# Performance work log

Measured on AMD Instinct MI355X. Metric: run time of the kernel, lower is better.

Reference implementation:

```python
import jax, jax.numpy as jnp
import numpy as np

N, E = 2048, 65536
EMBED, H0, H1 = 64, 128, 128
VOCAB = 625  # 5**k with k=4
SLOPE = 0.01  # F.leaky_relu_ default negative slope


def setup_inputs() -> dict:
    key = jax.random.key(0)
    ks = jax.random.split(key, 20)
    f = jax.random.normal
    return {
        "node_ids": jax.random.randint(ks[0], (N,), 0, VOCAB),
        "edge_index": jax.random.randint(ks[1], (2, E), 0, N),
        "edge_attr": jax.random.uniform(ks[2], (E, 1), dtype=jnp.float32),
        "m": (jax.random.uniform(ks[3], (N, N)) > 0.5).astype(jnp.float32),
        "emb": f(ks[4], (VOCAB, EMBED), dtype=jnp.float32) * 0.1,
        "l0_lin1": f(ks[5], (H0, EMBED + 1), dtype=jnp.float32) * 0.1,
        "l0_lin2": f(ks[6], (H0, H0), dtype=jnp.float32) * 0.1,
        "l0_att_l": f(ks[7], (H0,), dtype=jnp.float32) * 0.1,
        "l0_att_r": f(ks[8], (EMBED,), dtype=jnp.float32) * 0.1,
        "l0_bias": f(ks[9], (H0,), dtype=jnp.float32) * 0.1,
        "l1_lin1": f(ks[10], (H1, H0 + 1), dtype=jnp.float32) * 0.1,
        "l1_lin2": f(ks[11], (H1, H1), dtype=jnp.float32) * 0.1,
        "l1_att_l": f(ks[12], (H1,), dtype=jnp.float32) * 0.1,
        "l1_att_r": f(ks[13], (H0,), dtype=jnp.float32) * 0.1,
        "l1_bias": f(ks[14], (H1,), dtype=jnp.float32) * 0.1,
        "W1": f(ks[15], (20, (EMBED + H0 + H1) * 2), dtype=jnp.float32) * 0.1,
        "b1": f(ks[16], (20,), dtype=jnp.float32) * 0.1,
        "W2": f(ks[17], (20,), dtype=jnp.float32) * 0.1,
        "b2": f(ks[18], (1,), dtype=jnp.float32) * 0.1,
    }


def _segment_softmax(alpha, index, n):
    # numerically-stable softmax over edges grouped by destination node
    amax = jax.ops.segment_max(alpha, index, num_segments=n)
    amax = jnp.where(jnp.isfinite(amax), amax, 0.0)
    e = jnp.exp(alpha - amax[index])
    denom = jax.ops.segment_sum(e, index, num_segments=n)
    return e / (denom[index] + 1e-16)


def _gate_conv(x, src, dst, edge_attr, lin1, lin2, att_l, att_r, bias, n):
    # PyG AttentiveFP GATEConv: message = lin2(leaky_relu(lin1([x_j, e]))) * alpha
    h = jax.nn.leaky_relu(jnp.concatenate([x[src], edge_attr], axis=-1) @ lin1.T, SLOPE)  # [E,out]
    alpha = jax.nn.leaky_relu(h @ att_l + x[dst] @ att_r, SLOPE)  # [E]
    alpha = _segment_softmax(alpha, dst, n)
    msg = (h @ lin2.T) * alpha[:, None]
    return jax.ops.segment_sum(msg, dst, num_segments=n) + bias


def reference(node_ids, edge_index, edge_attr, m, emb,
              l0_lin1, l0_lin2, l0_att_l, l0_att_r, l0_bias,
              l1_lin1, l1_lin2, l1_att_l, l1_att_r, l1_bias,
              W1, b1, W2, b2):
    src, dst = edge_index[0], edge_index[1]
    x = emb[node_ids]  # [N, EMBED]
    h1 = jax.nn.relu(_gate_conv(x, src, dst, edge_attr, l0_lin1, l0_lin2, l0_att_l, l0_att_r, l0_bias, N))
    h2 = jax.nn.relu(_gate_conv(h1, src, dst, edge_attr, l1_lin1, l1_lin2, l1_att_l, l1_att_r, l1_bias, N))
    feat = jnp.concatenate([x, h1, h2], axis=-1)  # [N, C], C = EMBED+H0+H1
    C = feat.shape[-1]
    # 1x1 conv over concat([x_i, x_j]) == split linear: out[c,i,j] = W1[c,:C]@feat[i] + W1[c,C:]@feat[j] + b1[c]
    a = feat @ W1[:, :C].T  # [N, 20] row (i) term
    b = feat @ W1[:, C:].T  # [N, 20] col (j) term
    h = jax.nn.relu(a[:, None, :] + b[None, :, :] + b1)  # [N, N, 20]
    logits = (h @ W2 + b2[0]) * m  # [N, N]; mask multiplies logits as in original
    return jax.nn.softmax(logits, axis=1)
```

## Files before the change

### kernel.cpp

```cpp
#include <hip/hip_runtime.h>
#include <math.h>

#define N 2048
#define E 65536
#define EMBED 64
#define H 128
#define NT 20
#define C3 320
#define CAP 96
#define SLOPE 0.01f

__device__ __forceinline__ float leaky(float x) { return x > 0.f ? x : SLOPE * x; }

__device__ __forceinline__ float wave_sum(float v) {
#pragma unroll
    for (int o = 32; o > 0; o >>= 1) v += __shfl_xor(v, o, 64);
    return v;
}

__global__ __launch_bounds__(256) void k_prep(
    const int* __restrict__ ei, const float* __restrict__ eattr,
    int* __restrict__ cursor, int* __restrict__ srcs, float* __restrict__ eas,
    const float* __restrict__ l1_lin1, float* __restrict__ WT1,
    const float* __restrict__ l0_lin2, float* __restrict__ LT0,
    const float* __restrict__ l1_lin2, float* __restrict__ LT1,
    const int* __restrict__ ids, const float* __restrict__ emb,
    const float* __restrict__ l0_lin1,
    float* __restrict__ x, float* __restrict__ A) {
    int b = blockIdx.x;
    int tid = threadIdx.x;
    if (b < 256) {
        int e = b * 256 + tid;
        int d = ei[E + e];
        int pos = atomicAdd(&cursor[d], 1);
        if (pos < CAP) {
            srcs[d * CAP + pos] = ei[e];
            eas[d * CAP + pos] = eattr[e];
        }
    } else if (b < 448) {
        int j = (b - 256) * 256 + tid;
        if (j < 16384) {
            int c = j >> 7, k = j & 127;
            WT1[j] = l1_lin1[k * (H + 1) + c];
        } else if (j < 32768) {
            int jj = j - 16384; int c = jj >> 7, k = jj & 127;
            LT0[jj] = l0_lin2[k * H + c];
        } else {
            int jj = j - 32768; int c = jj >> 7, k = jj & 127;
            LT1[jj] = l1_lin2[k * H + c];
        }
    } else {
        __shared__ float lw[EMBED][130];
        int n0 = (b - 448) * 8;
        for (int j = tid; j < H * (EMBED + 1); j += 256) {
            int k = j / (EMBED + 1), c = j % (EMBED + 1);
            float v = l0_lin1[j];
            if (c < EMBED) lw[c][k] = v;
        }
        for (int idx = tid; idx < 8 * EMBED; idx += 256) {
            int g = idx >> 6, c = idx & 63;
            x[(n0 + g) * EMBED + c] = emb[ids[n0 + g] * EMBED + c];
        }
        __syncthreads();
        int k = tid & 127, half = tid >> 7;
        const float* xr[4];
#pragma unroll
        for (int it = 0; it < 4; it++) {
            int nn = __builtin_amdgcn_readfirstlane(n0 + 2 * it + half);
            xr[it] = emb + (size_t)ids[nn] * EMBED;
        }
        float acc[4] = {0.f, 0.f, 0.f, 0.f};
#pragma unroll 4
        for (int c = 0; c < EMBED; c++) {
            float wt = lw[c][k];
#pragma unroll
            for (int it = 0; it < 4; it++) acc[it] = fmaf(xr[it][c], wt, acc[it]);
        }
#pragma unroll
        for (int it = 0; it < 4; it++) A[(n0 + 2 * it + half) * H + k] = acc[it];
    }
}

__device__ __forceinline__ void gate_wave(
    int dst, int lane, float xr,
    const float* __restrict__ A,
    float w0, float w1, float attl0, float attl1,
    const int* __restrict__ srcs, const float* __restrict__ eas, int cnt,
    float& out0, float& out1) {
    int c0 = 2 * lane;
    int base = dst * CAP;
    float mmax = -INFINITY, s = 0.f, v0 = 0.f, v1 = 0.f;
    for (int i0 = 0; i0 < cnt; i0 += 8) {
        int nb = cnt - i0; if (nb > 8) nb = 8;
        float h0[8], h1[8], p[8];
#pragma unroll
        for (int e = 0; e < 8; e++) {
            float ea = 0.f; float2 av = make_float2(0.f, 0.f);
            if (e < nb) {
                int sn = srcs[base + i0 + e];
                ea = eas[base + i0 + e];
                av = *(const float2*)&A[sn * H + c0];
            }
            h0[e] = leaky(fmaf(w0, ea, av.x));
            h1[e] = leaky(fmaf(w1, ea, av.y));
            p[e] = h0[e] * attl0 + h1[e] * attl1;
        }
#pragma unroll
        for (int o = 32; o > 0; o >>= 1) {
#pragma unroll
            for (int e = 0; e < 8; e++) p[e] += __shfl_xor(p[e], o, 64);
        }
        float alpha[8];
#pragma unroll
        for (int e = 0; e < 8; e++)
            alpha[e] = (e < nb) ? leaky(p[e] + xr) : -INFINITY;
        float mb = alpha[0];
#pragma unroll
        for (int e = 1; e < 8; e++) mb = fmaxf(mb, alpha[e]);
        float mnew = fmaxf(mmax, mb);
        float scale = __expf(mmax - mnew);
        float sw = 0.f, sv0 = 0.f, sv1 = 0.f;
#pragma unroll
        for (int e = 0; e < 8; e++) {
            float we = __expf(alpha[e] - mnew);
            sw += we;
            sv0 = fmaf(we, h0[e], sv0);
            sv1 = fmaf(we, h1[e], sv1);
        }
        s = fmaf(s, scale, sw);
        v0 = fmaf(v0, scale, sv0);
        v1 = fmaf(v1, scale, sv1);
        mmax = mnew;
    }
    float inv = 1.f / (s + 1e-16f);
    out0 = v0 * inv;
    out1 = v1 * inv;
}

__global__ __launch_bounds__(512) void k_g0(
    const float* __restrict__ x, const float* __restrict__ A0,
    const float* __restrict__ l0_lin1,
    const float* __restrict__ att_l, const float* __restrict__ att_r,
    const int* __restrict__ srcs, const float* __restrict__ eas,
    const int* __restrict__ cursor,
    const float* __restrict__ LT0, const float* __restrict__ b0,
    const float* __restrict__ WT1,
    float* __restrict__ h1, float* __restrict__ A1) {
    __shared__ float agg_s[8][H];
    __shared__ float hs[8][H];
    int n0 = blockIdx.x * 8;
    int tid = threadIdx.x;
    int wv = __builtin_amdgcn_readfirstlane(tid >> 6);
    int lane = tid & 63;
    int c0 = 2 * lane;

    int dst = n0 + wv;
    float xr = wave_sum(x[dst * EMBED + lane] * att_r[lane]);
    float attl0 = att_l[c0], attl1 = att_l[c0 + 1];
    float w0 = l0_lin1[c0 * (EMBED + 1) + EMBED];
    float w1 = l0_lin1[(c0 + 1) * (EMBED + 1) + EMBED];
    int cnt = cursor[dst]; if (cnt > CAP) cnt = CAP;

    float o0, o1;
    gate_wave(dst, lane, xr, A0, w0, w1, attl0, attl1, srcs, eas, cnt, o0, o1);
    agg_s[wv][c0] = o0;
    agg_s[wv][c0 + 1] = o1;
    __syncthreads();

    int k = tid & 127, q = tid >> 7;
    float bk = b0[k];
    float acc0 = bk, acc1 = bk;
#pragma unroll 2
    for (int ct = 0; ct < H / 4; ct++) {
        float u0 = LT0[(4 * ct + 0) * H + k];
        float u1 = LT0[(4 * ct + 1) * H + k];
        float u2 = LT0[(4 * ct + 2) * H + k];
        float u3 = LT0[(4 * ct + 3) * H + k];
        float4 f0 = *(const float4*)&agg_s[q][4 * ct];
        float4 f1 = *(const float4*)&agg_s[q + 4][4 * ct];
        acc0 = fmaf(f0.x, u0, acc0); acc0 = fmaf(f0.y, u1, acc0);
        acc0 = fmaf(f0.z, u2, acc0); acc0 = fmaf(f0.w, u3, acc0);
        acc1 = fmaf(f1.x, u0, acc1); acc1 = fmaf(f1.y, u1, acc1);
        acc1 = fmaf(f1.z, u2, acc1); acc1 = fmaf(f1.w, u3, acc1);
    }
    float hv0 = fmaxf(acc0, 0.f), hv1 = fmaxf(acc1, 0.f);
    h1[(n0 + q) * H + k] = hv0;
    h1[(n0 + q + 4) * H + k] = hv1;
    hs[q][k] = hv0;
    hs[q + 4][k] = hv1;
    __syncthreads();

    float a0 = 0.f, a1 = 0.f;
#pragma unroll 2
    for (int ct = 0; ct < H / 4; ct++) {
        float u0 = WT1[(4 * ct + 0) * H + k];
        float u1 = WT1[(4 * ct + 1) * H + k];
        float u2 = WT1[(4 * ct + 2) * H + k];
        float u3 = WT1[(4 * ct + 3) * H + k];
        float4 f0 = *(const float4*)&hs[q][4 * ct];
        float4 f1 = *(const float4*)&hs[q + 4][4 * ct];
        a0 = fmaf(f0.x, u0, a0); a0 = fmaf(f0.y, u1, a0);
        a0 = fmaf(f0.z, u2, a0); a0 = fmaf(f0.w, u3, a0);
        a1 = fmaf(f1.x, u0, a1); a1 = fmaf(f1.y, u1, a1);
        a1 = fmaf(f1.z, u2, a1); a1 = fmaf(f1.w, u3, a1);
    }
    A1[(n0 + q) * H + k] = a0;
    A1[(n0 + q + 4) * H + k] = a1;
}

__global__ __launch_bounds__(512) void k_g1(
    const float* __restrict__ h1g, const float* __restrict__ A1,
    const float* __restrict__ l1_lin1,
    const float* __restrict__ att_l, const float* __restrict__ att_r,
    const int* __restrict__ srcs, const float* __restrict__ eas,
    const int* __restrict__ cursor,
    const float* __restrict__ LT1, const float* __restrict__ bL1,
    const float* __restrict__ x, const float* __restrict__ W1,
    float* __restrict__ aArr, float* __restrict__ bT) {
    __shared__ float agg_s[8][H];
    __shared__ float feat[8][C3];
    int n0 = blockIdx.x * 8;
    int tid = threadIdx.x;
    int wv = __builtin_amdgcn_readfirstlane(tid >> 6);
    int lane = tid & 63;
    int c0 = 2 * lane;

    int dst = n0 + wv;
    float xr = wave_sum(h1g[dst * H + lane] * att_r[lane] +
                        h1g[dst * H + 64 + lane] * att_r[64 + lane]);
    float attl0 = att_l[c0], attl1 = att_l[c0 + 1];
    float w0 = l1_lin1[c0 * (H + 1) + H];
    float w1 = l1_lin1[(c0 + 1) * (H + 1) + H];
    int cnt = cursor[dst]; if (cnt > CAP) cnt = CAP;

    float o0, o1;
    gate_wave(dst, lane, xr, A1, w0, w1, attl0, attl1, srcs, eas, cnt, o0, o1);
    agg_s[wv][c0] = o0;
    agg_s[wv][c0 + 1] = o1;

    for (int idx = tid; idx < 8 * EMBED; idx += 512) {
        int g = idx >> 6, c = idx & 63;
        feat[g][c] = x[(n0 + g) * EMBED + c];
    }
    for (int idx = tid; idx < 8 * H; idx += 512) {
        int g = idx >> 7, c = idx & 127;
        feat[g][EMBED + c] = h1g[(n0 + g) * H + c];
    }
    __syncthreads();

    int k = tid & 127, q = tid >> 7;
    float bk = bL1[k];
    float acc0 = bk, acc1 = bk;
#pragma unroll 2
    for (int ct = 0; ct < H / 4; ct++) {
        float u0 = LT1[(4 * ct + 0) * H + k];
        float u1 = LT1[(4 * ct + 1) * H + k];
        float u2 = LT1[(4 * ct + 2) * H + k];
        float u3 = LT1[(4 * ct + 3) * H + k];
        float4 f0 = *(const float4*)&agg_s[q][4 * ct];
        float4 f1 = *(const float4*)&agg_s[q + 4][4 * ct];
        acc0 = fmaf(f0.x, u0, acc0); acc0 = fmaf(f0.y, u1, acc0);
        acc0 = fmaf(f0.z, u2, acc0); acc0 = fmaf(f0.w, u3, acc0);
        acc1 = fmaf(f1.x, u0, acc1); acc1 = fmaf(f1.y, u1, acc1);
        acc1 = fmaf(f1.z, u2, acc1); acc1 = fmaf(f1.w, u3, acc1);
    }
    feat[q][EMBED + H + k] = fmaxf(acc0, 0.f);
    feat[q + 4][EMBED + H + k] = fmaxf(acc1, 0.f);
    __syncthreads();

    if (tid < 320) {
        int g = tid / 40, u = tid % 40;
        int t = u % 20, side = u / 20;
        const float* wrow = W1 + t * (2 * C3) + side * C3;
        float s = 0.f;
#pragma unroll 4
        for (int ct = 0; ct < C3 / 4; ct++) {
            float4 fv = *(const float4*)&feat[g][4 * ct];
            float4 wv4 = *(const float4*)&wrow[4 * ct];
            s = fmaf(fv.x, wv4.x, s);
            s = fmaf(fv.y, wv4.y, s);
            s = fmaf(fv.z, wv4.z, s);
            s = fmaf(fv.w, wv4.w, s);
        }
        if (side == 0) aArr[(n0 + g) * NT + t] = s;
        else bT[t * N + (n0 + g)] = s;
    }
}

__global__ __launch_bounds__(256) void k_final(const float* __restrict__ aArr,
                                               const float* __restrict__ bT,
                                               const float* __restrict__ b1,
                                               const float* __restrict__ W2,
                                               const float* __restrict__ b2,
                                               const float* __restrict__ mmat,
                                               float* __restrict__ out) {
    __shared__ float red[16];
    int i0 = blockIdx.x * 4;
    int tid = threadIdx.x;
    int lane = tid & 63, wv = tid >> 6;
    float w2r[NT];
#pragma unroll
    for (int t = 0; t < NT; t++) w2r[t] = W2[t];
    float b2v = b2[0];
    float ab[4][NT];
#pragma unroll
    for (int g = 0; g < 4; g++) {
#pragma unroll
        for (int t = 0; t < NT; t++)
            ab[g][t] = aArr[(i0 + g) * NT + t] + b1[t];
    }
    float l[4][8];
    float tmax[4] = {-INFINITY, -INFINITY, -INFINITY, -INFINITY};
#pragma unroll
    for (int it = 0; it < 8; it++) {
        int j = tid + 256 * it;
        float bt[NT];
#pragma unroll
        for (int t = 0; t < NT; t++) bt[t] = bT[t * N + j];
#pragma unroll
        for (int g = 0; g < 4; g++) {
            float s = b2v;
#pragma unroll
            for (int t = 0; t < NT; t++)
                s += fmaxf(ab[g][t] + bt[t], 0.f) * w2r[t];
            s *= mmat[(size_t)(i0 + g) * N + j];
            l[g][it] = s;
            tmax[g] = fmaxf(tmax[g], s);
        }
    }
#pragma unroll
    for (int g = 0; g < 4; g++) {
#pragma unroll
        for (int o = 32; o > 0; o >>= 1)
            tmax[g] = fmaxf(tmax[g], __shfl_xor(tmax[g], o, 64));
    }
    if (lane == 0) {
#pragma unroll
        for (int g = 0; g < 4; g++) red[wv * 4 + g] = tmax[g];
    }
    __syncthreads();
    float mfin[4];
#pragma unroll
    for (int g = 0; g < 4; g++)
        mfin[g] = fmaxf(fmaxf(red[g], red[4 + g]), fmaxf(red[8 + g], red[12 + g]));
    __syncthreads();

    float ts[4] = {0.f, 0.f, 0.f, 0.f};
#pragma unroll
    for (int it = 0; it < 8; it++) {
#pragma unroll
        for (int g = 0; g < 4; g++) {
            float e = __expf(l[g][it] - mfin[g]);
            l[g][it] = e;
            ts[g] += e;
        }
    }
#pragma unroll
    for (int g = 0; g < 4; g++) {
#pragma unroll
        for (int o = 32; o > 0; o >>= 1) ts[g] += __shfl_xor(ts[g], o, 64);
    }
    if (lane == 0) {
#pragma unroll
        for (int g = 0; g < 4; g++) red[wv * 4 + g] = ts[g];
    }
    __syncthreads();
    float inv[4];
#pragma unroll
    for (int g = 0; g < 4; g++)
        inv[g] = 1.f / (red[g] + red[4 + g] + red[8 + g] + red[12 + g]);

#pragma unroll
    for (int it = 0; it < 8; it++) {
        int j = tid + 256 * it;
#pragma unroll
        for (int g = 0; g < 4; g++)
            out[(size_t)(i0 + g) * N + j] = l[g][it] * inv[g];
    }
}

extern "C" void kernel_launch(void* const* d_in, const int* in_sizes, int n_in,
                              void* d_out, int out_size, void* d_ws, size_t ws_size,
                              hipStream_t stream) {
    const int*   node_ids = (const int*)d_in[0];
    const int*   ei       = (const int*)d_in[1];
    const float* eattr    = (const float*)d_in[2];
    const float* mmat     = (const float*)d_in[3];
    const float* emb      = (const float*)d_in[4];
    const float* l0_lin1  = (const float*)d_in[5];
    const float* l0_lin2  = (const float*)d_in[6];
    const float* l0_att_l = (const float*)d_in[7];
    const float* l0_att_r = (const float*)d_in[8];
    const float* l0_bias  = (const float*)d_in[9];
    const float* l1_lin1  = (const float*)d_in[10];
    const float* l1_lin2  = (const float*)d_in[11];
    const float* l1_att_l = (const float*)d_in[12];
    const float* l1_att_r = (const float*)d_in[13];
    const float* l1_bias  = (const float*)d_in[14];
    const float* W1       = (const float*)d_in[15];
    const float* b1       = (const float*)d_in[16];
    const float* W2       = (const float*)d_in[17];
    const float* b2       = (const float*)d_in[18];
    float* out = (float*)d_out;

    char* w = (char*)d_ws;
    auto alloc = [&](size_t bytes) {
        char* p = w;
        w += (bytes + 255) & ~(size_t)255;
        return p;
    };
    int*   cursor = (int*)alloc(N * sizeof(int));
    int*   srcs   = (int*)alloc(N * CAP * sizeof(int));
    float* eas    = (float*)alloc(N * CAP * sizeof(float));
    float* x      = (float*)alloc(N * EMBED * sizeof(float));
    float* A0     = (float*)alloc(N * H * sizeof(float));
    float* A1     = (float*)alloc(N * H * sizeof(float));
    float* h1     = (float*)alloc(N * H * sizeof(float));
    float* aArr   = (float*)alloc(N * NT * sizeof(float));
    float* bT     = (float*)alloc(NT * N * sizeof(float));
    float* WT1    = (float*)alloc(H * H * sizeof(float));
    float* LT0    = (float*)alloc(H * H * sizeof(float));
    float* LT1    = (float*)alloc(H * H * sizeof(float));

    hipMemsetAsync(cursor, 0, N * sizeof(int), stream);

    k_prep<<<704, 256, 0, stream>>>(ei, eattr, cursor, srcs, eas,
                                    l1_lin1, WT1, l0_lin2, LT0, l1_lin2, LT1,
                                    node_ids, emb, l0_lin1, x, A0);
    k_g0<<<N / 8, 512, 0, stream>>>(x, A0, l0_lin1, l0_att_l, l0_att_r,
                                    srcs, eas, cursor, LT0, l0_bias, WT1, h1, A1);
    k_g1<<<N / 8, 512, 0, stream>>>(h1, A1, l1_lin1, l1_att_l, l1_att_r,
                                    srcs, eas, cursor, LT1, l1_bias, x, W1, aArr, bT);
    k_final<<<N / 4, 256, 0, stream>>>(aArr, bT, b1, W2, b2, mmat, out);
}
```

Before: 185.8 us.

## Fuse all four kernels into one persistent kernel with software grid barriers

Replaces the prep, two gate-conv and final softmax kernels with a single 256-block persistent kernel. The stages are separated by atomic-counter grid barriers in global memory, and shared memory is reused across phases. The aim is to remove launch overhead and inter-kernel gaps. The trade-off is that only 256 blocks run, which may underfill the GPU in the final softmax phase (k_final used 512 blocks of 256 threads). Correctness also depends on all blocks being co-resident for the spin barrier.

```diff
diff --git a/kernel.cpp b/kernel.cpp
--- a/kernel.cpp
+++ b/kernel.cpp
@@ -9,6 +9,8 @@
 #define C3 320
 #define CAP 96
 #define SLOPE 0.01f
+#define NBLK 256
+#define NTHR 512
 
 __device__ __forceinline__ float leaky(float x) { return x > 0.f ? x : SLOPE * x; }
 
@@ -18,67 +20,16 @@
     return v;
 }
 
-__global__ __launch_bounds__(256) void k_prep(
-    const int* __restrict__ ei, const float* __restrict__ eattr,
-    int* __restrict__ cursor, int* __restrict__ srcs, float* __restrict__ eas,
-    const float* __restrict__ l1_lin1, float* __restrict__ WT1,
-    const float* __restrict__ l0_lin2, float* __restrict__ LT0,
-    const float* __restrict__ l1_lin2, float* __restrict__ LT1,
-    const int* __restrict__ ids, const float* __restrict__ emb,
-    const float* __restrict__ l0_lin1,
-    float* __restrict__ x, float* __restrict__ A) {
-    int b = blockIdx.x;
-    int tid = threadIdx.x;
-    if (b < 256) {
-        int e = b * 256 + tid;
-        int d = ei[E + e];
-        int pos = atomicAdd(&cursor[d], 1);
-        if (pos < CAP) {
-            srcs[d * CAP + pos] = ei[e];
-            eas[d * CAP + pos] = eattr[e];
-        }
-    } else if (b < 448) {
-        int j = (b - 256) * 256 + tid;
-        if (j < 16384) {
-            int c = j >> 7, k = j & 127;
-            WT1[j] = l1_lin1[k * (H + 1) + c];
-        } else if (j < 32768) {
-            int jj = j - 16384; int c = jj >> 7, k = jj & 127;
-            LT0[jj] = l0_lin2[k * H + c];
-        } else {
-            int jj = j - 32768; int c = jj >> 7, k = jj & 127;
-            LT1[jj] = l1_lin2[k * H + c];
-        }
-    } else {
-        __shared__ float lw[EMBED][130];
-        int n0 = (b - 448) * 8;
-        for (int j = tid; j < H * (EMBED + 1); j += 256) {
-            int k = j / (EMBED + 1), c = j % (EMBED + 1);
-            float v = l0_lin1[j];
-            if (c < EMBED) lw[c][k] = v;
-        }
-        for (int idx = tid; idx < 8 * EMBED; idx += 256) {
-            int g = idx >> 6, c = idx & 63;
-            x[(n0 + g) * EMBED + c] = emb[ids[n0 + g] * EMBED + c];
-        }
-        __syncthreads();
-        int k = tid & 127, half = tid >> 7;
-        const float* xr[4];
-#pragma unroll
-        for (int it = 0; it < 4; it++) {
-            int nn = __builtin_amdgcn_readfirstlane(n0 + 2 * it + half);
-            xr[it] = emb + (size_t)ids[nn] * EMBED;
-        }
-        float acc[4] = {0.f, 0.f, 0.f, 0.f};
-#pragma unroll 4
-        for (int c = 0; c < EMBED; c++) {
-            float wt = lw[c][k];
-#pragma unroll
-            for (int it = 0; it < 4; it++) acc[it] = fmaf(xr[it][c], wt, acc[it]);
-        }
-#pragma unroll
-        for (int it = 0; it < 4; it++) A[(n0 + 2 * it + half) * H + k] = acc[it];
-    }
+__device__ __forceinline__ void grid_sync(int* bar, int target) {
+    __syncthreads();
+    if (threadIdx.x == 0) {
+        __builtin_amdgcn_fence(__ATOMIC_RELEASE, "agent");
+        __hip_atomic_fetch_add(bar, 1, __ATOMIC_RELAXED, __HIP_MEMORY_SCOPE_AGENT);
+        while (__hip_atomic_load(bar, __ATOMIC_RELAXED, __HIP_MEMORY_SCOPE_AGENT) < target)
+            __builtin_amdgcn_s_sleep(2);
+        __builtin_amdgcn_fence(__ATOMIC_ACQUIRE, "agent");
+    }
+    __syncthreads();
 }
 
 __device__ __forceinline__ void gate_wave(
@@ -92,7 +43,7 @@
     float mmax = -INFINITY, s = 0.f, v0 = 0.f, v1 = 0.f;
     for (int i0 = 0; i0 < cnt; i0 += 8) {
         int nb = cnt - i0; if (nb > 8) nb = 8;
-        float h0[8], h1[8], p[8];
+        float h0[8], h1v[8], p[8];
 #pragma unroll
         for (int e = 0; e < 8; e++) {
             float ea = 0.f; float2 av = make_float2(0.f, 0.f);
@@ -102,8 +53,8 @@
                 av = *(const float2*)&A[sn * H + c0];
             }
             h0[e] = leaky(fmaf(w0, ea, av.x));
-            h1[e] = leaky(fmaf(w1, ea, av.y));
-            p[e] = h0[e] * attl0 + h1[e] * attl1;
+            h1v[e] = leaky(fmaf(w1, ea, av.y));
+            p[e] = h0[e] * attl0 + h1v[e] * attl1;
         }
 #pragma unroll
         for (int o = 32; o > 0; o >>= 1) {
@@ -125,7 +76,7 @@
             float we = __expf(alpha[e] - mnew);
             sw += we;
             sv0 = fmaf(we, h0[e], sv0);
-            sv1 = fmaf(we, h1[e], sv1);
+            sv1 = fmaf(we, h1v[e], sv1);
         }
         s = fmaf(s, scale, sw);
         v0 = fmaf(v0, scale, sv0);
@@ -137,245 +88,292 @@
     out1 = v1 * inv;
 }
 
-__global__ __launch_bounds__(512) void k_g0(
-    const float* __restrict__ x, const float* __restrict__ A0,
-    const float* __restrict__ l0_lin1,
-    const float* __restrict__ att_l, const float* __restrict__ att_r,
-    const int* __restrict__ srcs, const float* __restrict__ eas,
-    const int* __restrict__ cursor,
-    const float* __restrict__ LT0, const float* __restrict__ b0,
-    const float* __restrict__ WT1,
-    float* __restrict__ h1, float* __restrict__ A1) {
-    __shared__ float agg_s[8][H];
-    __shared__ float hs[8][H];
-    int n0 = blockIdx.x * 8;
-    int tid = threadIdx.x;
-    int wv = __builtin_amdgcn_readfirstlane(tid >> 6);
-    int lane = tid & 63;
-    int c0 = 2 * lane;
-
-    int dst = n0 + wv;
-    float xr = wave_sum(x[dst * EMBED + lane] * att_r[lane]);
-    float attl0 = att_l[c0], attl1 = att_l[c0 + 1];
-    float w0 = l0_lin1[c0 * (EMBED + 1) + EMBED];
-    float w1 = l0_lin1[(c0 + 1) * (EMBED + 1) + EMBED];
-    int cnt = cursor[dst]; if (cnt > CAP) cnt = CAP;
-
-    float o0, o1;
-    gate_wave(dst, lane, xr, A0, w0, w1, attl0, attl1, srcs, eas, cnt, o0, o1);
-    agg_s[wv][c0] = o0;
-    agg_s[wv][c0 + 1] = o1;
-    __syncthreads();
-
-    int k = tid & 127, q = tid >> 7;
-    float bk = b0[k];
-    float acc0 = bk, acc1 = bk;
+__global__ __launch_bounds__(NTHR) void k_fused(
+    const int* __restrict__ ids, const int* __restrict__ ei,
+    const float* __restrict__ eattr, const float* __restrict__ mmat,
+    const float* __restrict__ emb,
+    const float* __restrict__ l0_lin1, const float* __restrict__ l0_lin2,
+    const float* __restrict__ l0_att_l, const float* __restrict__ l0_att_r,
+    const float* __restrict__ l0_bias,
+    const float* __restrict__ l1_lin1, const float* __restrict__ l1_lin2,
+    const float* __restrict__ l1_att_l, const float* __restrict__ l1_att_r,
+    const float* __restrict__ l1_bias,
+    const float* __restrict__ W1, const float* __restrict__ b1,
+    const float* __restrict__ W2, const float* __restrict__ b2,
+    int* __restrict__ cursor, int* __restrict__ bar,
+    int* __restrict__ srcs, float* __restrict__ eas,
+    float* __restrict__ x, float* __restrict__ A0, float* __restrict__ A1,
+    float* __restrict__ h1, float* __restrict__ aArr, float* __restrict__ bT,
+    float* __restrict__ WT1, float* __restrict__ LT0, float* __restrict__ LT1,
+    float* __restrict__ out) {
+    __shared__ float smem[EMBED * 130];
+    const int b = blockIdx.x;
+    const int tid = threadIdx.x;
+    const int gtid = b * NTHR + tid;
+
+    if (gtid < E) {
+        int d = ei[E + gtid];
+        int pos = atomicAdd(&cursor[d], 1);
+        if (pos < CAP) {
+            srcs[d * CAP + pos] = ei[gtid];
+            eas[d * CAP + pos] = eattr[gtid];
+        }
+    } else if (gtid < E + 16384) {
+        int j = gtid - E;
+        WT1[j] = l1_lin1[(j & 127) * (H + 1) + (j >> 7)];
+    } else if (gtid < E + 32768) {
+        int j = gtid - (E + 16384);
+        LT0[j] = l0_lin2[(j & 127) * H + (j >> 7)];
+    } else if (gtid < E + 49152) {
+        int j = gtid - (E + 32768);
+        LT1[j] = l1_lin2[(j & 127) * H + (j >> 7)];
+    }
+    {
+        int g = gtid >> 6, c = gtid & 63;
+        x[gtid] = emb[ids[g] * EMBED + c];
+    }
+    {
+        float (*lw)[130] = (float(*)[130])smem;
+        for (int j = tid; j < H * (EMBED + 1); j += NTHR) {
+            int kk = j / (EMBED + 1), c = j % (EMBED + 1);
+            float v = l0_lin1[j];
+            if (c < EMBED) lw[c][kk] = v;
+        }
+        __syncthreads();
+        int n0 = b * 8;
+        int k = tid & 127, grp = tid >> 7;
+        int nnA = __builtin_amdgcn_readfirstlane(n0 + grp);
+        int nnB = __builtin_amdgcn_readfirstlane(n0 + grp + 4);
+        const float* xrA = emb + (size_t)ids[nnA] * EMBED;
+        const float* xrB = emb + (size_t)ids[nnB] * EMBED;
+        float accA = 0.f, accB = 0.f;
+#pragma unroll 4
+        for (int c = 0; c < EMBED; c++) {
+            float wt = lw[c][k];
+            accA = fmaf(xrA[c], wt, accA);
+            accB = fmaf(xrB[c], wt, accB);
+        }
+        A0[(n0 + grp) * H + k] = accA;
+        A0[(n0 + grp + 4) * H + k] = accB;
+    }
+    grid_sync(bar, NBLK);
+
+    {
+        float (*agg_s)[H] = (float(*)[H])smem;
+        float (*hs)[H] = (float(*)[H])(smem + 8 * H);
+        int n0 = b * 8;
+        int wv = __builtin_amdgcn_readfirstlane(tid >> 6);
+        int lane = tid & 63;
+        int c0 = 2 * lane;
+        int dst = n0 + wv;
+        float xr = wave_sum(x[dst * EMBED + lane] * l0_att_r[lane]);
+        float attl0 = l0_att_l[c0], attl1 = l0_att_l[c0 + 1];
+        float w0 = l0_lin1[c0 * (EMBED + 1) + EMBED];
+        float w1 = l0_lin1[(c0 + 1) * (EMBED + 1) + EMBED];
+        int cnt = cursor[dst]; if (cnt > CAP) cnt = CAP;
+
+        float o0, o1;
+        gate_wave(dst, lane, xr, A0, w0, w1, attl0, attl1, srcs, eas, cnt, o0, o1);
+        agg_s[wv][c0] = o0;
+        agg_s[wv][c0 + 1] = o1;
+        __syncthreads();
+
+        int k = tid & 127, q = tid >> 7;
+        float bk = l0_bias[k];
+        float acc0 = bk, acc1 = bk;
 #pragma unroll 2
-    for (int ct = 0; ct < H / 4; ct++) {
-        float u0 = LT0[(4 * ct + 0) * H + k];
-        float u1 = LT0[(4 * ct + 1) * H + k];
-        float u2 = LT0[(4 * ct + 2) * H + k];
-        float u3 = LT0[(4 * ct + 3) * H + k];
-        float4 f0 = *(const float4*)&agg_s[q][4 * ct];
-        float4 f1 = *(const float4*)&agg_s[q + 4][4 * ct];
-        acc0 = fmaf(f0.x, u0, acc0); acc0 = fmaf(f0.y, u1, acc0);
-        acc0 = fmaf(f0.z, u2, acc0); acc0 = fmaf(f0.w, u3, acc0);
-        acc1 = fmaf(f1.x, u0, acc1); acc1 = fmaf(f1.y, u1, acc1);
-        acc1 = fmaf(f1.z, u2, acc1); acc1 = fmaf(f1.w, u3, acc1);
-    }
-    float hv0 = fmaxf(acc0, 0.f), hv1 = fmaxf(acc1, 0.f);
-    h1[(n0 + q) * H + k] = hv0;
-    h1[(n0 + q + 4) * H + k] = hv1;
-    hs[q][k] = hv0;
-    hs[q + 4][k] = hv1;
-    __syncthreads();
-
-    float a0 = 0.f, a1 = 0.f;
+        for (int ct = 0; ct < H / 4; ct++) {
+            float u0 = LT0[(4 * ct + 0) * H + k];
+            float u1 = LT0[(4 * ct + 1) * H + k];
+            float u2 = LT0[(4 * ct + 2) * H + k];
+            float u3 = LT0[(4 * ct + 3) * H + k];
+            float4 f0 = *(const float4*)&agg_s[q][4 * ct];
+            float4 f1 = *(const float4*)&agg_s[q + 4][4 * ct];
+            acc0 = fmaf(f0.x, u0, acc0); acc0 = fmaf(f0.y, u1, acc0);
+            acc0 = fmaf(f0.z, u2, acc0); acc0 = fmaf(f0.w, u3, acc0);
+            acc1 = fmaf(f1.x, u0, acc1); acc1 = fmaf(f1.y, u1, acc1);
+            acc1 = fmaf(f1.z, u2, acc1); acc1 = fmaf(f1.w, u3, acc1);
+        }
+        float hv0 = fmaxf(acc0, 0.f), hv1 = fmaxf(acc1, 0.f);
+        h1[(n0 + q) * H + k] = hv0;
+        h1[(n0 + q + 4) * H + k] = hv1;
+        hs[q][k] = hv0;
+        hs[q + 4][k] = hv1;
+        __syncthreads();
+
+        float a0 = 0.f, a1 = 0.f;
 #pragma unroll 2
-    for (int ct = 0; ct < H / 4; ct++) {
-        float u0 = WT1[(4 * ct + 0) * H + k];
-        float u1 = WT1[(4 * ct + 1) * H + k];
-        float u2 = WT1[(4 * ct + 2) * H + k];
-        float u3 = WT1[(4 * ct + 3) * H + k];
-        float4 f0 = *(const float4*)&hs[q][4 * ct];
-        float4 f1 = *(const float4*)&hs[q + 4][4 * ct];
-        a0 = fmaf(f0.x, u0, a0); a0 = fmaf(f0.y, u1, a0);
-        a0 = fmaf(f0.z, u2, a0); a0 = fmaf(f0.w, u3, a0);
-        a1 = fmaf(f1.x, u0, a1); a1 = fmaf(f1.y, u1, a1);
-        a1 = fmaf(f1.z, u2, a1); a1 = fmaf(f1.w, u3, a1);
-    }
-    A1[(n0 + q) * H + k] = a0;
-    A1[(n0 + q + 4) * H + k] = a1;
-}
-
-__global__ __launch_bounds__(512) void k_g1(
-    const float* __restrict__ h1g, const float* __restrict__ A1,
-    const float* __restrict__ l1_lin1,
-    const float* __restrict__ att_l, const float* __restrict__ att_r,
-    const int* __restrict__ srcs, const float* __restrict__ eas,
-    const int* __restrict__ cursor,
-    const float* __restrict__ LT1, const float* __restrict__ bL1,
-    const float* __restrict__ x, const float* __restrict__ W1,
-    float* __restrict__ aArr, float* __restrict__ bT) {
-    __shared__ float agg_s[8][H];
-    __shared__ float feat[8][C3];
-    int n0 = blockIdx.x * 8;
-    int tid = threadIdx.x;
-    int wv = __builtin_amdgcn_readfirstlane(tid >> 6);
-    int lane = tid & 63;
-    int c0 = 2 * lane;
-
-    int dst = n0 + wv;
-    float xr = wave_sum(h1g[dst * H + lane] * att_r[lane] +
-                        h1g[dst * H + 64 + lane] * att_r[64 + lane]);
-    float attl0 = att_l[c0], attl1 = att_l[c0 + 1];
-    float w0 = l1_lin1[c0 * (H + 1) + H];
-    float w1 = l1_lin1[(c0 + 1) * (H + 1) + H];
-    int cnt = cursor[dst]; if (cnt > CAP) cnt = CAP;
-
-    float o0, o1;
-    gate_wave(dst, lane, xr, A1, w0, w1, attl0, attl1, srcs, eas, cnt, o0, o1);
-    agg_s[wv][c0] = o0;
-    agg_s[wv][c0 + 1] = o1;
-
-    for (int idx = tid; idx < 8 * EMBED; idx += 512) {
-        int g = idx >> 6, c = idx & 63;
-        feat[g][c] = x[(n0 + g) * EMBED + c];
-    }
-    for (int idx = tid; idx < 8 * H; idx += 512) {
-        int g = idx >> 7, c = idx & 127;
-        feat[g][EMBED + c] = h1g[(n0 + g) * H + c];
-    }
-    __syncthreads();
-
-    int k = tid & 127, q = tid >> 7;
-    float bk = bL1[k];
-    float acc0 = bk, acc1 = bk;
+        for (int ct = 0; ct < H / 4; ct++) {
+            float u0 = WT1[(4 * ct + 0) * H + k];
+            float u1 = WT1[(4 * ct + 1) * H + k];
+            float u2 = WT1[(4 * ct + 2) * H + k];
+            float u3 = WT1[(4 * ct + 3) * H + k];
+            float4 f0 = *(const float4*)&hs[q][4 * ct];
+            float4 f1 = *(const float4*)&hs[q + 4][4 * ct];
+            a0 = fmaf(f0.x, u0, a0); a0 = fmaf(f0.y, u1, a0);
+            a0 = fmaf(f0.z, u2, a0); a0 = fmaf(f0.w, u3, a0);
+            a1 = fmaf(f1.x, u0, a1); a1 = fmaf(f1.y, u1, a1);
+            a1 = fmaf(f1.z, u2, a1); a1 = fmaf(f1.w, u3, a1);
+        }
+        A1[(n0 + q) * H + k] = a0;
+        A1[(n0 + q + 4) * H + k] = a1;
+    }
+    grid_sync(bar, 2 * NBLK);
+
+    {
+        float (*agg_s)[H] = (float(*)[H])smem;
+        float (*feat)[C3] = (float(*)[C3])(smem + 8 * H);
+        int n0 = b * 8;
+        int wv = __builtin_amdgcn_readfirstlane(tid >> 6);
+        int lane = tid & 63;
+        int c0 = 2 * lane;
+        int dst = n0 + wv;
+        float xr = wave_sum(h1[dst * H + lane] * l1_att_r[lane] +
+                            h1[dst * H + 64 + lane] * l1_att_r[64 + lane]);
+        float attl0 = l1_att_l[c0], attl1 = l1_att_l[c0 + 1];
+        float w0 = l1_lin1[c0 * (H + 1) + H];
+        float w1 = l1_lin1[(c0 + 1) * (H + 1) + H];
+        int cnt = cursor[dst]; if (cnt > CAP) cnt = CAP;
+
+        float o0, o1;
+        gate_wave(dst, lane, xr, A1, w0, w1, attl0, attl1, srcs, eas, cnt, o0, o1);
+        agg_s[wv][c0] = o0;
+        agg_s[wv][c0 + 1] = o1;
+
+        for (int idx = tid; idx < 8 * EMBED; idx += NTHR) {
+            int g = idx >> 6, c = idx & 63;
+            feat[g][c] = x[(n0 + g) * EMBED + c];
+        }
+        for (int idx = tid; idx < 8 * H; idx += NTHR) {
+            int g = idx >> 7, c = idx & 127;
+            feat[g][EMBED + c] = h1[(n0 + g) * H + c];
+        }
+        __syncthreads();
+
+        int k = tid & 127, q = tid >> 7;
+        float bk = l1_bias[k];
+        float acc0 = bk, acc1 = bk;
 #pragma unroll 2
-    for (int ct = 0; ct < H / 4; ct++) {
-        float u0 = LT1[(4 * ct + 0) * H + k];
-        float u1 = LT1[(4 * ct + 1) * H + k];
-        float u2 = LT1[(4 * ct + 2) * H + k];
-        float u3 = LT1[(4 * ct + 3) * H + k];
-        float4 f0 = *(const float4*)&agg_s[q][4 * ct];
-        float4 f1 = *(const float4*)&agg_s[q + 4][4 * ct];
-        acc0 = fmaf(f0.x, u0, acc0); acc0 = fmaf(f0.y, u1, acc0);
-        acc0 = fmaf(f0.z, u2, acc0); acc0 = fmaf(f0.w, u3, acc0);
-        acc1 = fmaf(f1.x, u0, acc1); acc1 = fmaf(f1.y, u1, acc1);
-        acc1 = fmaf(f1.z, u2, acc1); acc1 = fmaf(f1.w, u3, acc1);
-    }
-    feat[q][EMBED + H + k] = fmaxf(acc0, 0.f);
-    feat[q + 4][EMBED + H + k] = fmaxf(acc1, 0.f);
-    __syncthreads();
-
-    if (tid < 320) {
-        int g = tid / 40, u = tid % 40;
-        int t = u % 20, side = u / 20;
-        const float* wrow = W1 + t * (2 * C3) + side * C3;
-        float s = 0.f;
+        for (int ct = 0; ct < H / 4; ct++) {
+            float u0 = LT1[(4 * ct + 0) * H + k];
+            float u1 = LT1[(4 * ct + 1) * H + k];
+            float u2 = LT1[(4 * ct + 2) * H + k];
+            float u3 = LT1[(4 * ct + 3) * H + k];
+            float4 f0 = *(const float4*)&agg_s[q][4 * ct];
+            float4 f1 = *(const float4*)&agg_s[q + 4][4 * ct];
+            acc0 = fmaf(f0.x, u0, acc0); acc0 = fmaf(f0.y, u1, acc0);
+            acc0 = fmaf(f0.z, u2, acc0); acc0 = fmaf(f0.w, u3, acc0);
+            acc1 = fmaf(f1.x, u0, acc1); acc1 = fmaf(f1.y, u1, acc1);
+            acc1 = fmaf(f1.z, u2, acc1); acc1 = fmaf(f1.w, u3, acc1);
+        }
+        feat[q][EMBED + H + k] = fmaxf(acc0, 0.f);
+        feat[q + 4][EMBED + H + k] = fmaxf(acc1, 0.f);
+        __syncthreads();
+
+        if (tid < 320) {
+            int g = tid / 40, u = tid % 40;
+            int t = u % 20, side = u / 20;
+            const float* wrow = W1 + t * (2 * C3) + side * C3;
+            float s = 0.f;
 #pragma unroll 4
-        for (int ct = 0; ct < C3 / 4; ct++) {
-            float4 fv = *(const float4*)&feat[g][4 * ct];
-            float4 wv4 = *(const float4*)&wrow[4 * ct];
-            s = fmaf(fv.x, wv4.x, s);
-            s = fmaf(fv.y, wv4.y, s);
-            s = fmaf(fv.z, wv4.z, s);
-            s = fmaf(fv.w, wv4.w, s);
-        }
-        if (side == 0) aArr[(n0 + g) * NT + t] = s;
-        else bT[t * N + (n0 + g)] = s;
-    }
-}
-
-__global__ __launch_bounds__(256) void k_final(const float* __restrict__ aArr,
-                                               const float* __restrict__ bT,
-                                               const float* __restrict__ b1,
-                                               const float* __restrict__ W2,
-                                               const float* __restrict__ b2,
-                                               const float* __restrict__ mmat,
-                                               float* __restrict__ out) {
-    __shared__ float red[16];
-    int i0 = blockIdx.x * 4;
-    int tid = threadIdx.x;
-    int lane = tid & 63, wv = tid >> 6;
-    float w2r[NT];
-#pragma unroll
-    for (int t = 0; t < NT; t++) w2r[t] = W2[t];
-    float b2v = b2[0];
-    float ab[4][NT];
-#pragma unroll
-    for (int g = 0; g < 4; g++) {
-#pragma unroll
-        for (int t = 0; t < NT; t++)
-            ab[g][t] = aArr[(i0 + g) * NT + t] + b1[t];
-    }
-    float l[4][8];
-    float tmax[4] = {-INFINITY, -INFINITY, -INFINITY, -INFINITY};
-#pragma unroll
-    for (int it = 0; it < 8; it++) {
-        int j = tid + 256 * it;
-        float bt[NT];
-#pragma unroll
-        for (int t = 0; t < NT; t++) bt[t] = bT[t * N + j];
+            for (int ct = 0; ct < C3 / 4; ct++) {
+                float4 fv = *(const float4*)&feat[g][4 * ct];
+                float4 wv4 = *(const float4*)&wrow[4 * ct];
+                s = fmaf(fv.x, wv4.x, s);
+                s = fmaf(fv.y, wv4.y, s);
+                s = fmaf(fv.z, wv4.z, s);
+                s = fmaf(fv.w, wv4.w, s);
+            }
+            if (side == 0) aArr[(n0 + g) * NT + t] = s;
+            else bT[t * N + (n0 + g)] = s;
+        }
+    }
+    grid_sync(bar, 3 * NBLK);
+
+    {
+        float* red = smem + (tid >> 8) * 16;
+        int t256 = tid & 255;
+        int i0 = b * 8 + (tid >> 8) * 4;
+        int lane = t256 & 63, wv = t256 >> 6;
+        float w2r[NT];
+#pragma unroll
+        for (int t = 0; t < NT; t++) w2r[t] = W2[t];
+        float b2v = b2[0];
+        float ab[4][NT];
 #pragma unroll
         for (int g = 0; g < 4; g++) {
-            float s = b2v;
 #pragma unroll
             for (int t = 0; t < NT; t++)
-                s += fmaxf(ab[g][t] + bt[t], 0.f) * w2r[t];
-            s *= mmat[(size_t)(i0 + g) * N + j];
-            l[g][it] = s;
-            tmax[g] = fmaxf(tmax[g], s);
-        }
-    }
-#pragma unroll
-    for (int g = 0; g < 4; g++) {
-#pragma unroll
-        for (int o = 32; o > 0; o >>= 1)
-            tmax[g] = fmaxf(tmax[g], __shfl_xor(tmax[g], o, 64));
-    }
-    if (lane == 0) {
-#pragma unroll
-        for (int g = 0; g < 4; g++) red[wv * 4 + g] = tmax[g];
-    }
-    __syncthreads();
-    float mfin[4];
-#pragma unroll
-    for (int g = 0; g < 4; g++)
-        mfin[g] = fmaxf(fmaxf(red[g], red[4 + g]), fmaxf(red[8 + g], red[12 + g]));
-    __syncthreads();
-
-    float ts[4] = {0.f, 0.f, 0.f, 0.f};
-#pragma unroll
-    for (int it = 0; it < 8; it++) {
+                ab[g][t] = aArr[(i0 + g) * NT + t] + b1[t];
+        }
+        float l[4][8];
+        float tmax[4] = {-INFINITY, -INFINITY, -INFINITY, -INFINITY};
+#pragma unroll
+        for (int it = 0; it < 8; it++) {
+            int j = t256 + 256 * it;
+            float bt[NT];
+#pragma unroll
+            for (int t = 0; t < NT; t++) bt[t] = bT[t * N + j];
+#pragma unroll
+            for (int g = 0; g < 4; g++) {
+                float s = b2v;
+#pragma unroll
+                for (int t = 0; t < NT; t++)
+                    s += fmaxf(ab[g][t] + bt[t], 0.f) * w2r[t];
+                s *= mmat[(size_t)(i0 + g) * N + j];
+                l[g][it] = s;
+                tmax[g] = fmaxf(tmax[g], s);
+            }
+        }
 #pragma unroll
         for (int g = 0; g < 4; g++) {
-            float e = __expf(l[g][it] - mfin[g]);
-            l[g][it] = e;
-            ts[g] += e;
-        }
-    }
-#pragma unroll
-    for (int g = 0; g < 4; g++) {
-#pragma unroll
-        for (int o = 32; o > 0; o >>= 1) ts[g] += __shfl_xor(ts[g], o, 64);
-    }
-    if (lane == 0) {
-#pragma unroll
-        for (int g = 0; g < 4; g++) red[wv * 4 + g] = ts[g];
-    }
-    __syncthreads();
-    float inv[4];
-#pragma unroll
-    for (int g = 0; g < 4; g++)
-        inv[g] = 1.f / (red[g] + red[4 + g] + red[8 + g] + red[12 + g]);
-
-#pragma unroll
-    for (int it = 0; it < 8; it++) {
-        int j = tid + 256 * it;
+#pragma unroll
+            for (int o = 32; o > 0; o >>= 1)
+                tmax[g] = fmaxf(tmax[g], __shfl_xor(tmax[g], o, 64));
+        }
+        if (lane == 0) {
+#pragma unroll
+            for (int g = 0; g < 4; g++) red[wv * 4 + g] = tmax[g];
+        }
+        __syncthreads();
+        float mfin[4];
 #pragma unroll
         for (int g = 0; g < 4; g++)
-            out[(size_t)(i0 + g) * N + j] = l[g][it] * inv[g];
+            mfin[g] = fmaxf(fmaxf(red[g], red[4 + g]), fmaxf(red[8 + g], red[12 + g]));
+        __syncthreads();
+
+        float ts[4] = {0.f, 0.f, 0.f, 0.f};
+#pragma unroll
+        for (int it = 0; it < 8; it++) {
+#pragma unroll
+            for (int g = 0; g < 4; g++) {
+                float e = __expf(l[g][it] - mfin[g]);
+                l[g][it] = e;
+                ts[g] += e;
+            }
+        }
+#pragma unroll
+        for (int g = 0; g < 4; g++) {
+#pragma unroll
+            for (int o = 32; o > 0; o >>= 1) ts[g] += __shfl_xor(ts[g], o, 64);
+        }
+        if (lane == 0) {
+#pragma unroll
+            for (int g = 0; g < 4; g++) red[wv * 4 + g] = ts[g];
+        }
+        __syncthreads();
+        float inv[4];
+#pragma unroll
+        for (int g = 0; g < 4; g++)
+            inv[g] = 1.f / (red[g] + red[4 + g] + red[8 + g] + red[12 + g]);
+
+#pragma unroll
+        for (int it = 0; it < 8; it++) {
+            int j = t256 + 256 * it;
+#pragma unroll
+            for (int g = 0; g < 4; g++)
+                out[(size_t)(i0 + g) * N + j] = l[g][it] * inv[g];
+        }
     }
 }
 
@@ -409,7 +407,8 @@
         w += (bytes + 255) & ~(size_t)255;
         return p;
     };
-    int*   cursor = (int*)alloc(N * sizeof(int));
+    int*   cursor = (int*)alloc((N + 64) * sizeof(int));
+    int*   bar    = cursor + N;
     int*   srcs   = (int*)alloc(N * CAP * sizeof(int));
     float* eas    = (float*)alloc(N * CAP * sizeof(float));
     float* x      = (float*)alloc(N * EMBED * sizeof(float));
@@ -422,14 +421,12 @@
     float* LT0    = (float*)alloc(H * H * sizeof(float));
     float* LT1    = (float*)alloc(H * H * sizeof(float));
 
-    hipMemsetAsync(cursor, 0, N * sizeof(int), stream);
-
-    k_prep<<<704, 256, 0, stream>>>(ei, eattr, cursor, srcs, eas,
-                                    l1_lin1, WT1, l0_lin2, LT0, l1_lin2, LT1,
-                                    node_ids, emb, l0_lin1, x, A0);
-    k_g0<<<N / 8, 512, 0, stream>>>(x, A0, l0_lin1, l0_att_l, l0_att_r,
-                                    srcs, eas, cursor, LT0, l0_bias, WT1, h1, A1);
-    k_g1<<<N / 8, 512, 0, stream>>>(h1, A1, l1_lin1, l1_att_l, l1_att_r,
-                                    srcs, eas, cursor, LT1, l1_bias, x, W1, aArr, bT);
-    k_final<<<N / 4, 256, 0, stream>>>(aArr, bT, b1, W2, b2, mmat, out);
+    hipMemsetAsync(cursor, 0, (N + 64) * sizeof(int), stream);
+
+    k_fused<<<NBLK, NTHR, 0, stream>>>(node_ids, ei, eattr, mmat, emb,
+                                       l0_lin1, l0_lin2, l0_att_l, l0_att_r, l0_bias,
+                                       l1_lin1, l1_lin2, l1_att_l, l1_att_r, l1_bias,
+                                       W1, b1, W2, b2,
+                                       cursor, bar, srcs, eas, x, A0, A1, h1,
+                                       aArr, bT, WT1, LT0, LT1, out);
 }
```

After: 220.2 us. 1.19x slower.
